# Optimization experiments

Hardware: AMD Instinct MI355X
Metric: run time of the kernel (lower is better)

## Reference

```python
import jax, jax.numpy as jnp
import numpy as np

D_MODEL = 512
NUM_HEADS = 8
HEAD_DIM = D_MODEL // NUM_HEADS


def setup_inputs() -> dict:
    key = jax.random.key(0)
    k1, k2, k3, k4, k5 = jax.random.split(key, 5)
    B, S = 4, 2048
    hidden_states = jax.random.normal(k1, (B, S, D_MODEL), dtype=jnp.float32)
    attention_mask = jnp.ones((B, S), dtype=jnp.int32)
    scale = 1.0 / np.sqrt(D_MODEL)
    Wq = jax.random.normal(k2, (D_MODEL, D_MODEL), dtype=jnp.float32) * scale
    Wk = jax.random.normal(k3, (D_MODEL, D_MODEL), dtype=jnp.float32) * scale
    Wv = jax.random.normal(k4, (D_MODEL, D_MODEL), dtype=jnp.float32) * scale
    Wo = jax.random.normal(k5, (D_MODEL, D_MODEL), dtype=jnp.float32) * scale
    return {
        "hidden_states": hidden_states,
        "attention_mask": attention_mask,
        "Wq": Wq, "Wk": Wk, "Wv": Wv, "Wo": Wo,
        "window_size": 256,
    }


def reference(hidden_states, attention_mask, Wq, Wk, Wv, Wo, window_size):
    B, S, _ = hidden_states.shape
    H, Dh = NUM_HEADS, HEAD_DIM
    # torch Linear: y = x @ W.T  (weights are [out, in])
    q = (hidden_states @ Wq.T).reshape(B, S, H, Dh).transpose(0, 2, 1, 3)
    k = (hidden_states @ Wk.T).reshape(B, S, H, Dh).transpose(0, 2, 1, 3)
    v = (hidden_states @ Wv.T).reshape(B, S, H, Dh).transpose(0, 2, 1, 3)
    scores = jnp.einsum('bhnd,bhmd->bhnm', q, k) / jnp.sqrt(jnp.float32(Dh))
    # tril(diagonal=window_size-1): allow key m iff m - n <= window_size - 1
    n = jnp.arange(S)[:, None]
    m = jnp.arange(S)[None, :]
    band = (m - n) <= (window_size - 1)  # [S, S]
    allowed = band[None, None, :, :] & (attention_mask[:, None, None, :] != 0)
    scores = jnp.where(allowed, scores, -jnp.inf)
    attn = jax.nn.softmax(scores, axis=-1)
    out = jnp.einsum('bhnm,bhmd->bhnd', attn, v)
    out = out.transpose(0, 2, 1, 3).reshape(B, S, H * Dh)
    return out @ Wo.T
```

## Files before the change

### kernel.cpp

```cpp
#include <hip/hip_runtime.h>
#include <hip/hip_bf16.h>

#define BATCH 4
#define SEQ 2048
#define DM 512
#define NH 8
#define DH 64
#define WINDOW 256
#define NEGINF (-1e30f)
#define C_SCALE 0.18033688f
#define THR2 11.5415603f

typedef __attribute__((ext_vector_type(8)))  short bf16x8;
typedef __attribute__((ext_vector_type(4)))  float f32x4;
typedef __attribute__((ext_vector_type(16))) float f32x16;

__device__ __forceinline__ unsigned short f2bf(float f) {
    __hip_bfloat16 h = __float2bfloat16(f);
    union { __hip_bfloat16 h; unsigned short u; } cv; cv.h = h; return cv.u;
}
__device__ __forceinline__ unsigned int pack2(float a, float b) {
    return (unsigned int)f2bf(a) | ((unsigned int)f2bf(b) << 16);
}

__device__ __forceinline__ int swz128(int row, int byte_in_row) {
    return row * 128 + (byte_in_row ^ ((row & 7) << 4));
}

#define MFMA(a, b, c)   __builtin_amdgcn_mfma_f32_16x16x32_bf16(a, b, c, 0, 0, 0)
#define MFMA32(a, b, c) __builtin_amdgcn_mfma_f32_32x32x16_bf16(a, b, c, 0, 0, 0)

__global__ __launch_bounds__(256) void cvt8_w(
    const float* __restrict__ W0, const float* __restrict__ W1,
    const float* __restrict__ W2, const float* __restrict__ W3,
    unsigned short* __restrict__ out, int n8) {
    const float* in = (blockIdx.y == 0) ? W0 : (blockIdx.y == 1) ? W1
                    : (blockIdx.y == 2) ? W2 : W3;
    unsigned short* o = out + (size_t)blockIdx.y * n8 * 8;
    int i = blockIdx.x * 256 + threadIdx.x;
    if (i >= n8) return;
    const float4* p = (const float4*)in + 2 * (size_t)i;
    float4 a = p[0], b = p[1];
    union { unsigned short s[8]; uint4 v; } u;
    u.s[0] = f2bf(a.x); u.s[1] = f2bf(a.y); u.s[2] = f2bf(a.z); u.s[3] = f2bf(a.w);
    u.s[4] = f2bf(b.x); u.s[5] = f2bf(b.y); u.s[6] = f2bf(b.z); u.s[7] = f2bf(b.w);
    *reinterpret_cast<uint4*>(o + 8 * (size_t)i) = u.v;
}

__global__ __launch_bounds__(256) void gemm_qkv(
    const float* __restrict__ A,
    const unsigned short* __restrict__ Wbase,
    unsigned short* __restrict__ C0, unsigned short* __restrict__ C1,
    unsigned short* __restrict__ C2, int M, int N, int K, int vtz)
{
    const unsigned short* W = Wbase + (size_t)blockIdx.z * N * K;
    unsigned short* C = (blockIdx.z == 0) ? C0 : (blockIdx.z == 1) ? C1 : C2;

    __shared__ unsigned short SMEM[128 * 136];
    unsigned short* As = SMEM;
    unsigned short* Ws = SMEM + 128 * 64;

    const int tid  = threadIdx.x;
    const int m0   = blockIdx.x * 128;
    const int n0   = blockIdx.y * 128;
    const int lane = tid & 63;
    const int wv   = tid >> 6;
    const int wm   = wv >> 1, wn = wv & 1;
    const int g    = lane >> 4;
    const int lr   = lane & 15;
    const int r0   = tid >> 2;
    const int cgrp = tid & 3;

    f32x4 acc[4][4];
#pragma unroll
    for (int i = 0; i < 4; ++i)
#pragma unroll
        for (int j = 0; j < 4; ++j) { f32x4 z = {0.f,0.f,0.f,0.f}; acc[i][j] = z; }

    float4 paf[2][4];
    uint4  pw[2][2];
    auto issue = [&](int k0) {
#pragma unroll
        for (int rr = 0; rr < 2; ++rr) {
            const float* sa = A + (size_t)(m0 + r0 + 64 * rr) * K + k0 + cgrp * 16;
#pragma unroll
            for (int c = 0; c < 4; ++c)
                paf[rr][c] = *reinterpret_cast<const float4*>(sa + 4 * c);
            const unsigned short* sw = W + (size_t)(n0 + r0 + 64 * rr) * K + k0 + cgrp * 16;
            pw[rr][0] = *reinterpret_cast<const uint4*>(sw);
            pw[rr][1] = *reinterpret_cast<const uint4*>(sw + 8);
        }
    };
    issue(0);

    for (int k0 = 0; k0 < K; k0 += 64) {
        __syncthreads();
#pragma unroll
        for (int rr = 0; rr < 2; ++rr) {
            const int r = r0 + 64 * rr;
#pragma unroll
            for (int c = 0; c < 4; ++c) {
                const float4 v = paf[rr][c];
                uint2 w; w.x = pack2(v.x, v.y); w.y = pack2(v.z, v.w);
                *reinterpret_cast<uint2*>((char*)As + swz128(r, cgrp * 32 + 8 * c)) = w;
            }
            *reinterpret_cast<uint4*>((char*)Ws + swz128(r, cgrp * 32))      = pw[rr][0];
            *reinterpret_cast<uint4*>((char*)Ws + swz128(r, cgrp * 32 + 16)) = pw[rr][1];
        }
        __syncthreads();
        if (k0 + 64 < K) issue(k0 + 64);

#pragma unroll
        for (int ks = 0; ks < 2; ++ks) {
            bf16x8 af[4], bfr[4];
#pragma unroll
            for (int i = 0; i < 4; ++i)
                af[i] = *reinterpret_cast<const bf16x8*>(
                    (char*)As + swz128(64 * wm + 16 * i + lr, 64 * ks + 16 * g));
#pragma unroll
            for (int j = 0; j < 4; ++j)
                bfr[j] = *reinterpret_cast<const bf16x8*>(
                    (char*)Ws + swz128(64 * wn + 16 * j + lr, 64 * ks + 16 * g));
#pragma unroll
            for (int i = 0; i < 4; ++i)
#pragma unroll
                for (int j = 0; j < 4; ++j)
                    acc[i][j] = MFMA(af[i], bfr[j], acc[i][j]);
        }
    }

    if ((int)blockIdx.z == vtz) {
        __syncthreads();
        unsigned short* T = SMEM;
#pragma unroll
        for (int i = 0; i < 4; ++i)
#pragma unroll
            for (int j = 0; j < 4; ++j) {
                const int col  = 64 * wn + 16 * j + lr;
                const int rowb = 64 * wm + 16 * i + 4 * g;
                uint2 v;
                v.x = pack2(acc[i][j][0], acc[i][j][1]);
                v.y = pack2(acc[i][j][2], acc[i][j][3]);
                *reinterpret_cast<uint2*>(&T[col * 136 + rowb]) = v;
            }
        __syncthreads();
        const int col = tid >> 1, hf = tid & 1;
        const int bb  = m0 >> 11;
        unsigned short* dst = C + ((size_t)bb * DM + n0 + col) * SEQ
                                + (m0 & (SEQ - 1)) + 64 * hf;
        const unsigned short* src = &T[col * 136 + 64 * hf];
#pragma unroll
        for (int c = 0; c < 8; ++c)
            *reinterpret_cast<uint4*>(dst + 8 * c) =
                *reinterpret_cast<const uint4*>(src + 8 * c);
        return;
    }

#pragma unroll
    for (int i = 0; i < 4; ++i)
#pragma unroll
        for (int j = 0; j < 4; ++j) {
            const int col = n0 + 64 * wn + 16 * j + lr;
#pragma unroll
            for (int r = 0; r < 4; ++r) {
                const int row = m0 + 64 * wm + 16 * i + 4 * g + r;
                C[(size_t)row * N + col] = f2bf(acc[i][j][r]);
            }
        }
}

__global__ __launch_bounds__(256) void gemm_out(
    const unsigned short* __restrict__ A,
    const unsigned short* __restrict__ W,
    float* __restrict__ C, int M, int N, int K)
{
    __shared__ unsigned short As[128 * 64];
    __shared__ unsigned short Ws[64 * 64];

    const int tid  = threadIdx.x;
    const int m0   = blockIdx.x * 128;
    const int n0   = blockIdx.y * 64;
    const int lane = tid & 63;
    const int wv   = tid >> 6;
    const int g    = lane >> 4;
    const int lr   = lane & 15;
    const int r0   = tid >> 2;
    const int cgrp = tid & 3;

    f32x4 acc[2][4];
#pragma unroll
    for (int i = 0; i < 2; ++i)
#pragma unroll
        for (int j = 0; j < 4; ++j) { f32x4 z = {0.f,0.f,0.f,0.f}; acc[i][j] = z; }

    uint4 pa[2][2], pw[2];
    auto issue = [&](int k0) {
#pragma unroll
        for (int rr = 0; rr < 2; ++rr) {
            const unsigned short* sa = A + (size_t)(m0 + r0 + 64 * rr) * K + k0 + cgrp * 16;
            pa[rr][0] = *reinterpret_cast<const uint4*>(sa);
            pa[rr][1] = *reinterpret_cast<const uint4*>(sa + 8);
        }
        const unsigned short* sw = W + (size_t)(n0 + r0) * K + k0 + cgrp * 16;
        pw[0] = *reinterpret_cast<const uint4*>(sw);
        pw[1] = *reinterpret_cast<const uint4*>(sw + 8);
    };
    issue(0);

    for (int k0 = 0; k0 < K; k0 += 64) {
        __syncthreads();
#pragma unroll
        for (int rr = 0; rr < 2; ++rr) {
            const int r = r0 + 64 * rr;
            *reinterpret_cast<uint4*>((char*)As + swz128(r, cgrp * 32))      = pa[rr][0];
            *reinterpret_cast<uint4*>((char*)As + swz128(r, cgrp * 32 + 16)) = pa[rr][1];
        }
        *reinterpret_cast<uint4*>((char*)Ws + swz128(r0, cgrp * 32))      = pw[0];
        *reinterpret_cast<uint4*>((char*)Ws + swz128(r0, cgrp * 32 + 16)) = pw[1];
        __syncthreads();
        if (k0 + 64 < K) issue(k0 + 64);

#pragma unroll
        for (int ks = 0; ks < 2; ++ks) {
            bf16x8 af[2], bfr[4];
#pragma unroll
            for (int i = 0; i < 2; ++i)
                af[i] = *reinterpret_cast<const bf16x8*>(
                    (char*)As + swz128(32 * wv + 16 * i + lr, 64 * ks + 16 * g));
#pragma unroll
            for (int j = 0; j < 4; ++j)
                bfr[j] = *reinterpret_cast<const bf16x8*>(
                    (char*)Ws + swz128(16 * j + lr, 64 * ks + 16 * g));
#pragma unroll
            for (int i = 0; i < 2; ++i)
#pragma unroll
                for (int j = 0; j < 4; ++j)
                    acc[i][j] = MFMA(af[i], bfr[j], acc[i][j]);
        }
    }

#pragma unroll
    for (int i = 0; i < 2; ++i)
#pragma unroll
        for (int j = 0; j < 4; ++j) {
            const int col = n0 + 16 * j + lr;
#pragma unroll
            for (int r = 0; r < 4; ++r) {
                const int row = m0 + 32 * wv + 16 * i + 4 * g + r;
                C[(size_t)row * N + col] = acc[i][j][r];
            }
        }
}

__global__ __launch_bounds__(256) void attn_mfma32(
    const unsigned short* __restrict__ Q, const unsigned short* __restrict__ K,
    const unsigned short* __restrict__ VtG, const int* __restrict__ amask,
    unsigned short* __restrict__ AO)
{
    __shared__ unsigned short Ks[2][64 * 64];
    __shared__ unsigned short Vt[2][64 * 64];

    const int tid = threadIdx.x;
    const int x   = (int)blockIdx.x;
    const int r_  = (x < 256) ? x : 767 - x;
    const int qb  = 15 - (r_ >> 5);
    const int bh  = r_ & 31;
    const int n0  = qb * 128;
    const int b = bh >> 3, h = bh & 7;

    const int lane = tid & 63;
    const int wv   = tid >> 6;
    const int ql   = lane & 31;
    const int hb   = lane >> 5;

    const int qrow  = n0 + 32 * wv + ql;
    const int qminw = n0 + 32 * wv;
    const int qmaxw = qminw + 31;

    bf16x8 qf[4];
    {
        const unsigned short* qp =
            Q + (size_t)(b * SEQ + qrow) * DM + h * DH + 8 * hb;
#pragma unroll
        for (int st = 0; st < 4; ++st)
            qf[st] = *reinterpret_cast<const bf16x8*>(qp + 16 * st);
    }

    f32x16 o[2];
#pragma unroll
    for (int i = 0; i < 16; ++i) { o[0][i] = 0.f; o[1][i] = 0.f; }
    float m_run = NEGINF, l_run = 0.f;

    int ntiles = (n0 + 127 + WINDOW - 1) / 64 + 1;
    if (ntiles > SEQ / 64) ntiles = SEQ / 64;

    const int r_st = tid & 63;
    const int half = tid >> 6;
    const int vd   = tid >> 2;
    const int vc   = (tid & 3) * 8;
    const unsigned short* kpt = K + (size_t)(b * SEQ + r_st) * DM + h * DH + 16 * half;
    const unsigned short* vpt = VtG + ((size_t)b * DM + h * DH + vd) * SEQ + vc;
    const int* amp = amask + (size_t)b * SEQ + r_st;

    uint4 kr0, kr1, vv0, vv1; int mr = 1;
    auto issue = [&](int tt) {
        const unsigned short* kp = kpt + (size_t)tt * 64 * DM;
        kr0 = *reinterpret_cast<const uint4*>(kp);
        kr1 = *reinterpret_cast<const uint4*>(kp + 8);
        const unsigned short* vp = vpt + tt * 64;
        vv0 = *reinterpret_cast<const uint4*>(vp);
        vv1 = *reinterpret_cast<const uint4*>(vp + 32);
        mr = amp[tt * 64];
    };
    auto writeKV = [&](int buf) {
        *reinterpret_cast<uint4*>((char*)Ks[buf] + swz128(r_st, 32 * half))      = kr0;
        *reinterpret_cast<uint4*>((char*)Ks[buf] + swz128(r_st, 32 * half + 16)) = kr1;
        *reinterpret_cast<uint4*>((char*)Vt[buf] + swz128(vd, 2 * vc))           = vv0;
        *reinterpret_cast<uint4*>((char*)Vt[buf] + swz128(vd, 2 * vc + 64))      = vv1;
    };

    unsigned long long mw0 = ~0ULL, mw1 = ~0ULL;

    issue(0);
    writeKV(0);
    mw0 = __ballot(mr != 0);
    issue(1);

    for (int t = 0; t < ntiles; ++t) {
        const int cur = t & 1;
        const int kv0 = t * 64;
        __syncthreads();
        if (t + 1 < ntiles) {
            writeKV(cur ^ 1);
            const unsigned long long bw = __ballot(mr != 0);
            if (cur == 0) mw1 = bw; else mw0 = bw;
        }
        if (t + 2 < ntiles) issue(t + 2);

        if (kv0 > qmaxw + (WINDOW - 1)) continue;

        const unsigned long long mwt = cur ? mw1 : mw0;
        const bool fullband =
            ((kv0 + 63 - qminw) <= (WINDOW - 1)) && (mwt == ~0ULL);

        f32x16 s[2];
        __builtin_amdgcn_s_setprio(1);
#pragma unroll
        for (int T = 0; T < 2; ++T) {
            f32x16 z;
#pragma unroll
            for (int i = 0; i < 16; ++i) z[i] = 0.f;
#pragma unroll
            for (int st = 0; st < 4; ++st) {
                bf16x8 kf = *reinterpret_cast<const bf16x8*>(
                    (char*)Ks[cur] + swz128(32 * T + ql, 32 * st + 16 * hb));
                z = MFMA32(kf, qf[st], z);
            }
            s[T] = z;
        }
        __builtin_amdgcn_s_setprio(0);

        if (!fullband) {
            const int lim = qrow + (WINDOW - 1) - kv0;
#pragma unroll
            for (int T = 0; T < 2; ++T)
#pragma unroll
                for (int rg = 0; rg < 16; ++rg) {
                    const int kvi = 32 * T + (rg & 3) + 8 * (rg >> 2) + 4 * hb;
                    const bool ok = (kvi <= lim) && ((mwt >> kvi) & 1ULL);
                    s[T][rg] = ok ? s[T][rg] : NEGINF;
                }
        }

        float tmax = NEGINF;
#pragma unroll
        for (int T = 0; T < 2; ++T)
#pragma unroll
            for (int rg = 0; rg < 16; ++rg) tmax = fmaxf(tmax, s[T][rg]);
        tmax = fmaxf(tmax, __shfl_xor(tmax, 32));
        const float tm2 = tmax * C_SCALE;

        if (!__all(tm2 - m_run <= THR2)) {
            const float mn = fmaxf(m_run, tm2);
            const float sc = exp2f(m_run - mn);
            m_run = mn; l_run *= sc;
#pragma unroll
            for (int rg = 0; rg < 16; ++rg) { o[0][rg] *= sc; o[1][rg] *= sc; }
        }

        float ls = 0.f;
        unsigned int pw[16];
#pragma unroll
        for (int T = 0; T < 2; ++T)
#pragma unroll
            for (int i = 0; i < 8; ++i) {
                const float p0 = exp2f(fmaf(s[T][2 * i],     C_SCALE, -m_run));
                const float p1 = exp2f(fmaf(s[T][2 * i + 1], C_SCALE, -m_run));
                ls += p0 + p1;
                unsigned int r;
                asm("v_cvt_pk_bf16_f32 %0, %1, %2" : "=v"(r) : "v"(p0), "v"(p1));
                pw[8 * T + i] = r;
            }
        ls += __shfl_xor(ls, 32);
        l_run += ls;

        __builtin_amdgcn_s_setprio(1);
#pragma unroll
        for (int c = 0; c < 4; ++c) {
            const int base = 8 * (c >> 1) + 4 * (c & 1);
            unsigned int a0 = pw[base],     b0 = pw[base + 2];
            unsigned int a1 = pw[base + 1], b1 = pw[base + 3];
            asm("v_permlane32_swap_b32 %0, %1" : "+v"(a0), "+v"(b0));
            asm("v_permlane32_swap_b32 %0, %1" : "+v"(a1), "+v"(b1));
            union { unsigned int w[4]; bf16x8 v; } pf;
            pf.w[0] = a0; pf.w[1] = a1; pf.w[2] = b0; pf.w[3] = b1;
#pragma unroll
            for (int dt = 0; dt < 2; ++dt) {
                bf16x8 vf = *reinterpret_cast<const bf16x8*>(
                    (char*)Vt[cur] + swz128(32 * dt + ql, 32 * c + 16 * hb));
                o[dt] = MFMA32(vf, pf.v, o[dt]);
            }
        }
        __builtin_amdgcn_s_setprio(0);
    }

    const float inv = 1.f / l_run;
    unsigned short* op = AO + (size_t)(b * SEQ + qrow) * DM + h * DH;
#pragma unroll
    for (int dt = 0; dt < 2; ++dt)
#pragma unroll
        for (int p = 0; p < 4; ++p) {
            const float f0 = o[dt][4 * p]     * inv, f1 = o[dt][4 * p + 1] * inv;
            const float f2 = o[dt][4 * p + 2] * inv, f3 = o[dt][4 * p + 3] * inv;
            unsigned int w0, w1;
            asm("v_cvt_pk_bf16_f32 %0, %1, %2" : "=v"(w0) : "v"(f0), "v"(f1));
            asm("v_cvt_pk_bf16_f32 %0, %1, %2" : "=v"(w1) : "v"(f2), "v"(f3));
            uint2 st; st.x = w0; st.y = w1;
            *reinterpret_cast<uint2*>(op + 32 * dt + 8 * p + 4 * hb) = st;
        }
}

extern "C" void kernel_launch(void* const* d_in, const int* in_sizes, int n_in,
                              void* d_out, int out_size, void* d_ws, size_t ws_size,
                              hipStream_t stream) {
    const float* hs    = (const float*)d_in[0];
    const int*   amask = (const int*)  d_in[1];
    const float* Wq    = (const float*)d_in[2];
    const float* Wk    = (const float*)d_in[3];
    const float* Wv    = (const float*)d_in[4];
    const float* Wo    = (const float*)d_in[5];
    float* out = (float*)d_out;

    const size_t tok = (size_t)BATCH * SEQ * DM;
    const size_t wsz = (size_t)DM * DM;
    unsigned short* Qb  = (unsigned short*)d_ws;
    unsigned short* Kb  = Qb + tok;
    unsigned short* VtG = Kb + tok;
    unsigned short* AOb = VtG + tok;
    unsigned short* Wb  = AOb + tok;

    const int M = BATCH * SEQ;

    cvt8_w<<<dim3((int)(wsz / 8 / 256), 4), 256, 0, stream>>>(
        Wq, Wk, Wv, Wo, Wb, (int)(wsz / 8));

    dim3 gQKV(M / 128, DM / 128, 3);
    gemm_qkv<<<gQKV, 256, 0, stream>>>(hs, Wb, Qb, Kb, VtG, M, DM, DM, 2);

    attn_mfma32<<<dim3(512), 256, 0, stream>>>(Qb, Kb, VtG, amask, AOb);

    dim3 gOut(M / 128, DM / 64);
    gemm_out<<<gOut, 256, 0, stream>>>(AOb, Wb + 3 * wsz, out, M, DM, DM);
}
```

Baseline: 137.8 us.

## Drop weight-conversion kernel and double-buffer LDS in projection GEMMs

Removes the separate fp32-to-bf16 weight conversion launch; both GEMMs now read fp32 weights directly and convert them while staging into LDS. The GEMM main loops move to double-buffered shared memory with a two-deep register prefetch, so only one barrier per k-step is needed and the LDS writes for the next tile overlap the MFMA work on the current one. Launch bounds now request two blocks per CU. In exchange, weight global traffic doubles per tile and conversion work is repeated by every block, and LDS use per block grows.

```diff
diff --git a/kernel.cpp b/kernel.cpp
--- a/kernel.cpp
+++ b/kernel.cpp
@@ -30,35 +30,17 @@
 #define MFMA(a, b, c)   __builtin_amdgcn_mfma_f32_16x16x32_bf16(a, b, c, 0, 0, 0)
 #define MFMA32(a, b, c) __builtin_amdgcn_mfma_f32_32x32x16_bf16(a, b, c, 0, 0, 0)
 
-__global__ __launch_bounds__(256) void cvt8_w(
-    const float* __restrict__ W0, const float* __restrict__ W1,
-    const float* __restrict__ W2, const float* __restrict__ W3,
-    unsigned short* __restrict__ out, int n8) {
-    const float* in = (blockIdx.y == 0) ? W0 : (blockIdx.y == 1) ? W1
-                    : (blockIdx.y == 2) ? W2 : W3;
-    unsigned short* o = out + (size_t)blockIdx.y * n8 * 8;
-    int i = blockIdx.x * 256 + threadIdx.x;
-    if (i >= n8) return;
-    const float4* p = (const float4*)in + 2 * (size_t)i;
-    float4 a = p[0], b = p[1];
-    union { unsigned short s[8]; uint4 v; } u;
-    u.s[0] = f2bf(a.x); u.s[1] = f2bf(a.y); u.s[2] = f2bf(a.z); u.s[3] = f2bf(a.w);
-    u.s[4] = f2bf(b.x); u.s[5] = f2bf(b.y); u.s[6] = f2bf(b.z); u.s[7] = f2bf(b.w);
-    *reinterpret_cast<uint4*>(o + 8 * (size_t)i) = u.v;
-}
-
-__global__ __launch_bounds__(256) void gemm_qkv(
+__global__ __launch_bounds__(256, 2) void gemm_qkv(
     const float* __restrict__ A,
-    const unsigned short* __restrict__ Wbase,
+    const float* __restrict__ W0f, const float* __restrict__ W1f,
+    const float* __restrict__ W2f,
     unsigned short* __restrict__ C0, unsigned short* __restrict__ C1,
     unsigned short* __restrict__ C2, int M, int N, int K, int vtz)
 {
-    const unsigned short* W = Wbase + (size_t)blockIdx.z * N * K;
+    const float* W = (blockIdx.z == 0) ? W0f : (blockIdx.z == 1) ? W1f : W2f;
     unsigned short* C = (blockIdx.z == 0) ? C0 : (blockIdx.z == 1) ? C1 : C2;
 
-    __shared__ unsigned short SMEM[128 * 136];
-    unsigned short* As = SMEM;
-    unsigned short* Ws = SMEM + 128 * 64;
+    __shared__ unsigned short SMEM[2 * 2 * 128 * 64];
 
     const int tid  = threadIdx.x;
     const int m0   = blockIdx.x * 128;
@@ -70,6 +52,7 @@
     const int lr   = lane & 15;
     const int r0   = tid >> 2;
     const int cgrp = tid & 3;
+    const int NIT  = K / 64;
 
     f32x4 acc[4][4];
 #pragma unroll
@@ -77,39 +60,50 @@
 #pragma unroll
         for (int j = 0; j < 4; ++j) { f32x4 z = {0.f,0.f,0.f,0.f}; acc[i][j] = z; }
 
-    float4 paf[2][4];
-    uint4  pw[2][2];
-    auto issue = [&](int k0) {
+    float4 pa[2][4], pwf[2][4];
+    auto issue = [&](int it) {
+        const int k0 = it * 64;
 #pragma unroll
         for (int rr = 0; rr < 2; ++rr) {
             const float* sa = A + (size_t)(m0 + r0 + 64 * rr) * K + k0 + cgrp * 16;
-#pragma unroll
-            for (int c = 0; c < 4; ++c)
-                paf[rr][c] = *reinterpret_cast<const float4*>(sa + 4 * c);
-            const unsigned short* sw = W + (size_t)(n0 + r0 + 64 * rr) * K + k0 + cgrp * 16;
-            pw[rr][0] = *reinterpret_cast<const uint4*>(sw);
-            pw[rr][1] = *reinterpret_cast<const uint4*>(sw + 8);
-        }
-    };
-    issue(0);
-
-    for (int k0 = 0; k0 < K; k0 += 64) {
-        __syncthreads();
+            const float* sw = W + (size_t)(n0 + r0 + 64 * rr) * K + k0 + cgrp * 16;
+#pragma unroll
+            for (int c = 0; c < 4; ++c) {
+                pa[rr][c]  = *reinterpret_cast<const float4*>(sa + 4 * c);
+                pwf[rr][c] = *reinterpret_cast<const float4*>(sw + 4 * c);
+            }
+        }
+    };
+    auto writeLDS = [&](int buf) {
+        unsigned short* As = SMEM + buf * 2 * 128 * 64;
+        unsigned short* Ws = As + 128 * 64;
 #pragma unroll
         for (int rr = 0; rr < 2; ++rr) {
             const int r = r0 + 64 * rr;
 #pragma unroll
             for (int c = 0; c < 4; ++c) {
-                const float4 v = paf[rr][c];
-                uint2 w; w.x = pack2(v.x, v.y); w.y = pack2(v.z, v.w);
-                *reinterpret_cast<uint2*>((char*)As + swz128(r, cgrp * 32 + 8 * c)) = w;
-            }
-            *reinterpret_cast<uint4*>((char*)Ws + swz128(r, cgrp * 32))      = pw[rr][0];
-            *reinterpret_cast<uint4*>((char*)Ws + swz128(r, cgrp * 32 + 16)) = pw[rr][1];
-        }
+                const float4 va = pa[rr][c];
+                uint2 wa; wa.x = pack2(va.x, va.y); wa.y = pack2(va.z, va.w);
+                *reinterpret_cast<uint2*>((char*)As + swz128(r, cgrp * 32 + 8 * c)) = wa;
+                const float4 vw = pwf[rr][c];
+                uint2 ww; ww.x = pack2(vw.x, vw.y); ww.y = pack2(vw.z, vw.w);
+                *reinterpret_cast<uint2*>((char*)Ws + swz128(r, cgrp * 32 + 8 * c)) = ww;
+            }
+        }
+    };
+
+    issue(0);
+    writeLDS(0);
+    issue(1);
+
+    for (int it = 0; it < NIT; ++it) {
+        const int cur = it & 1;
         __syncthreads();
-        if (k0 + 64 < K) issue(k0 + 64);
-
+        if (it + 1 < NIT) writeLDS(cur ^ 1);
+        if (it + 2 < NIT) issue(it + 2);
+
+        const unsigned short* As = SMEM + cur * 2 * 128 * 64;
+        const unsigned short* Ws = As + 128 * 64;
 #pragma unroll
         for (int ks = 0; ks < 2; ++ks) {
             bf16x8 af[4], bfr[4];
@@ -169,13 +163,12 @@
         }
 }
 
-__global__ __launch_bounds__(256) void gemm_out(
+__global__ __launch_bounds__(256, 2) void gemm_out(
     const unsigned short* __restrict__ A,
-    const unsigned short* __restrict__ W,
+    const float* __restrict__ Wf,
     float* __restrict__ C, int M, int N, int K)
 {
-    __shared__ unsigned short As[128 * 64];
-    __shared__ unsigned short Ws[64 * 64];
+    __shared__ unsigned short SMEM[2 * (128 * 64 + 64 * 64)];
 
     const int tid  = threadIdx.x;
     const int m0   = blockIdx.x * 128;
@@ -186,6 +179,7 @@
     const int lr   = lane & 15;
     const int r0   = tid >> 2;
     const int cgrp = tid & 3;
+    const int NIT  = K / 64;
 
     f32x4 acc[2][4];
 #pragma unroll
@@ -193,33 +187,51 @@
 #pragma unroll
         for (int j = 0; j < 4; ++j) { f32x4 z = {0.f,0.f,0.f,0.f}; acc[i][j] = z; }
 
-    uint4 pa[2][2], pw[2];
-    auto issue = [&](int k0) {
+    uint4  pa[2][2];
+    float4 pwf[4];
+    auto issue = [&](int it) {
+        const int k0 = it * 64;
 #pragma unroll
         for (int rr = 0; rr < 2; ++rr) {
-            const unsigned short* sa = A + (size_t)(m0 + r0 + 64 * rr) * K + k0 + cgrp * 16;
+            const unsigned short* sa =
+                A + (size_t)(m0 + r0 + 64 * rr) * K + k0 + cgrp * 16;
             pa[rr][0] = *reinterpret_cast<const uint4*>(sa);
             pa[rr][1] = *reinterpret_cast<const uint4*>(sa + 8);
         }
-        const unsigned short* sw = W + (size_t)(n0 + r0) * K + k0 + cgrp * 16;
-        pw[0] = *reinterpret_cast<const uint4*>(sw);
-        pw[1] = *reinterpret_cast<const uint4*>(sw + 8);
-    };
-    issue(0);
-
-    for (int k0 = 0; k0 < K; k0 += 64) {
-        __syncthreads();
+        const float* sw = Wf + (size_t)(n0 + r0) * K + k0 + cgrp * 16;
+#pragma unroll
+        for (int c = 0; c < 4; ++c)
+            pwf[c] = *reinterpret_cast<const float4*>(sw + 4 * c);
+    };
+    auto writeLDS = [&](int buf) {
+        unsigned short* As = SMEM + buf * (128 * 64 + 64 * 64);
+        unsigned short* Ws = As + 128 * 64;
 #pragma unroll
         for (int rr = 0; rr < 2; ++rr) {
             const int r = r0 + 64 * rr;
             *reinterpret_cast<uint4*>((char*)As + swz128(r, cgrp * 32))      = pa[rr][0];
             *reinterpret_cast<uint4*>((char*)As + swz128(r, cgrp * 32 + 16)) = pa[rr][1];
         }
-        *reinterpret_cast<uint4*>((char*)Ws + swz128(r0, cgrp * 32))      = pw[0];
-        *reinterpret_cast<uint4*>((char*)Ws + swz128(r0, cgrp * 32 + 16)) = pw[1];
+#pragma unroll
+        for (int c = 0; c < 4; ++c) {
+            const float4 vw = pwf[c];
+            uint2 ww; ww.x = pack2(vw.x, vw.y); ww.y = pack2(vw.z, vw.w);
+            *reinterpret_cast<uint2*>((char*)Ws + swz128(r0, cgrp * 32 + 8 * c)) = ww;
+        }
+    };
+
+    issue(0);
+    writeLDS(0);
+    issue(1);
+
+    for (int it = 0; it < NIT; ++it) {
+        const int cur = it & 1;
         __syncthreads();
-        if (k0 + 64 < K) issue(k0 + 64);
-
+        if (it + 1 < NIT) writeLDS(cur ^ 1);
+        if (it + 2 < NIT) issue(it + 2);
+
+        const unsigned short* As = SMEM + cur * (128 * 64 + 64 * 64);
+        const unsigned short* Ws = As + 128 * 64;
 #pragma unroll
         for (int ks = 0; ks < 2; ++ks) {
             bf16x8 af[2], bfr[4];
@@ -452,23 +464,18 @@
     float* out = (float*)d_out;
 
     const size_t tok = (size_t)BATCH * SEQ * DM;
-    const size_t wsz = (size_t)DM * DM;
     unsigned short* Qb  = (unsigned short*)d_ws;
     unsigned short* Kb  = Qb + tok;
     unsigned short* VtG = Kb + tok;
     unsigned short* AOb = VtG + tok;
-    unsigned short* Wb  = AOb + tok;
 
     const int M = BATCH * SEQ;
 
-    cvt8_w<<<dim3((int)(wsz / 8 / 256), 4), 256, 0, stream>>>(
-        Wq, Wk, Wv, Wo, Wb, (int)(wsz / 8));
-
     dim3 gQKV(M / 128, DM / 128, 3);
-    gemm_qkv<<<gQKV, 256, 0, stream>>>(hs, Wb, Qb, Kb, VtG, M, DM, DM, 2);
+    gemm_qkv<<<gQKV, 256, 0, stream>>>(hs, Wq, Wk, Wv, Qb, Kb, VtG, M, DM, DM, 2);
 
     attn_mfma32<<<dim3(512), 256, 0, stream>>>(Qb, Kb, VtG, amask, AOb);
 
     dim3 gOut(M / 128, DM / 64);
-    gemm_out<<<gOut, 256, 0, stream>>>(AOb, Wb + 3 * wsz, out, M, DM, DM);
-}
+    gemm_out<<<gOut, 256, 0, stream>>>(AOb, Wo, out, M, DM, DM);
+}
```

Measured after the change: 116.0 us (median of 5 runs). 15.8% less time.
